# Optimization experiments

Hardware: AMD Instinct MI355X
Metric: run time of the kernel (lower is better)

## Reference

```python
import jax, jax.numpy as jnp
import numpy as np

D, H, DFF, N = 256, 8, 2048, 100
B, T, M1, M2 = 64, 77, 400, 400
DH = D // H
EPS = 1e-5
NEG = -1e9


def _ln(x, w, b):
    m = jnp.mean(x, axis=-1, keepdims=True)
    v = jnp.mean((x - m) ** 2, axis=-1, keepdims=True)
    return (x - m) / jnp.sqrt(v + EPS) * w + b


def _mha(q_in, kv_in, in_w, in_b, out_w, out_b, kpm):
    # q_in: [Tq, D], kv_in: [Tk, D], in_w: [3D, D], kpm: [Tk] bool (True = pad)
    wq, wk, wv = in_w[:D], in_w[D:2 * D], in_w[2 * D:]
    bq, bk, bv = in_b[:D], in_b[D:2 * D], in_b[2 * D:]
    q = (q_in @ wq.T + bq).reshape(-1, H, DH)
    k = (kv_in @ wk.T + bk).reshape(-1, H, DH)
    v = (kv_in @ wv.T + bv).reshape(-1, H, DH)
    scores = jnp.einsum('qhd,khd->hqk', q, k) / np.sqrt(DH).astype(np.float32)
    scores = jnp.where(kpm[None, None, :], NEG, scores)
    attn = jax.nn.softmax(scores, axis=-1)
    out = jnp.einsum('hqk,khd->qhd', attn, v).reshape(-1, D)
    return out @ out_w.T + out_b


def _decoder(x, mem, tmask, mmask, saw, sab, saow, saob,
             caw, cab, caow, caob, l1w, l1b, l2w, l2b,
             n1w, n1b, n2w, n2b, n3w, n3b):
    # Post-norm TransformerDecoderLayer (eval mode, no dropout)
    x = _ln(x + _mha(x, x, saw, sab, saow, saob, tmask), n1w, n1b)
    x = _ln(x + _mha(x, mem, caw, cab, caow, caob, mmask), n2w, n2b)
    ff = jax.nn.relu(x @ l1w.T + l1b) @ l2w.T + l2b
    return _ln(x + ff, n3w, n3b)


def setup_inputs() -> dict:
    key = jax.random.key(0)
    ks = jax.random.split(key, 12)
    s = 0.02
    return {
        'text_embed': jax.random.normal(ks[0], (B, T, D), jnp.float32),
        'text_mask': jnp.zeros((B, T), bool),
        'im_embed1': jax.random.normal(ks[1], (B, M1, D), jnp.float32),
        'im_mask1': jnp.zeros((B, M1), bool),
        'im_embed2': jax.random.normal(ks[2], (B, M2, D), jnp.float32),
        'im_mask2': jnp.zeros((B, M2), bool),
        'sid': jax.random.randint(ks[3], (B,), 0, N),
        'sa_in_w': jax.random.normal(ks[4], (N, 3 * D, D), jnp.float32) * s,
        'sa_in_b': jnp.zeros((N, 3 * D), jnp.float32),
        'sa_out_w': jax.random.normal(ks[5], (N, D, D), jnp.float32) * s,
        'sa_out_b': jnp.zeros((N, D), jnp.float32),
        'ca_in_w': jax.random.normal(ks[6], (N, 3 * D, D), jnp.float32) * s,
        'ca_in_b': jnp.zeros((N, 3 * D), jnp.float32),
        'ca_out_w': jax.random.normal(ks[7], (N, D, D), jnp.float32) * s,
        'ca_out_b': jnp.zeros((N, D), jnp.float32),
        'lin1_w': jax.random.normal(ks[8], (N, DFF, D), jnp.float32) * s,
        'lin1_b': jnp.zeros((N, DFF), jnp.float32),
        'lin2_w': jax.random.normal(ks[9], (N, D, DFF), jnp.float32) * s,
        'lin2_b': jnp.zeros((N, D), jnp.float32),
        'ln1_w': jnp.ones((N, D), jnp.float32),
        'ln1_b': jnp.zeros((N, D), jnp.float32),
        'ln2_w': jnp.ones((N, D), jnp.float32),
        'ln2_b': jnp.zeros((N, D), jnp.float32),
        'ln3_w': jnp.ones((N, D), jnp.float32),
        'ln3_b': jnp.zeros((N, D), jnp.float32),
    }


def reference(text_embed, text_mask, im_embed1, im_mask1, im_embed2, im_mask2, sid,
              sa_in_w, sa_in_b, sa_out_w, sa_out_b,
              ca_in_w, ca_in_b, ca_out_w, ca_out_b,
              lin1_w, lin1_b, lin2_w, lin2_b,
              ln1_w, ln1_b, ln2_w, ln2_b, ln3_w, ln3_b):
    mem = jnp.concatenate([im_embed1, im_embed2], axis=1)    # [B, M1+M2, D]
    mmask = jnp.concatenate([im_mask1, im_mask2], axis=1)    # [B, M1+M2]
    params = tuple(p[sid] for p in (
        sa_in_w, sa_in_b, sa_out_w, sa_out_b,
        ca_in_w, ca_in_b, ca_out_w, ca_out_b,
        lin1_w, lin1_b, lin2_w, lin2_b,
        ln1_w, ln1_b, ln2_w, ln2_b, ln3_w, ln3_b))
    return jax.vmap(_decoder)(text_embed, mem, text_mask, mmask, *params)
```

## Files before the change

kernel.cpp:

```cpp
#include <hip/hip_runtime.h>
#include <hip/hip_bf16.h>
#include <math.h>

constexpr int kB   = 64;
constexpr int kT   = 77;
constexpr int kD   = 256;
constexpr int kH   = 8;
constexpr int kDH  = 32;
constexpr int kDFF = 2048;
constexpr int kM1  = 400;
constexpr int kMKV = 800;
constexpr float kEPS = 1e-5f;
constexpr float kNEG = -1000000000.0f;

typedef __attribute__((ext_vector_type(8))) short short8;
typedef __attribute__((ext_vector_type(4))) float floatx4;

__device__ __forceinline__ unsigned pkbf(float x, float y) {
    unsigned ux = __float_as_uint(x), uy = __float_as_uint(y);
    ux = (ux + 0x7fffu + ((ux >> 16) & 1u)) >> 16;
    uy = (uy + 0x7fffu + ((uy >> 16) & 1u)) & 0xffff0000u;
    return ux | uy;
}

__global__ __launch_bounds__(256) void mfma_gemm(
    const float* __restrict__ A1, long long sA1,
    const float* __restrict__ A2, long long sA2, int splitM, int lda,
    const float* __restrict__ W, long long sW, int ldw,
    const float* __restrict__ bias, long long sB,
    float* __restrict__ C, long long sC, int ldc,
    const int* __restrict__ sid, int M, int N, int K, int tilesM, int relu)
{
    __shared__ unsigned short As[128][88];
    __shared__ unsigned short Bs[128][88];

    int b = blockIdx.z;
    int s = sid[b];
    int ty = blockIdx.x % tilesM;
    int tx = blockIdx.x / tilesM;
    int tm0 = ty * 128, tn0 = tx * 128;

    const float* Wb = W + (long long)s * sW;
    const float* Bb = bias + (long long)s * sB;
    float* Cb = C + (long long)b * sC;

    int t = threadIdx.x;
    int lane = t & 63, wv = t >> 6;
    int wm = wv >> 1, wn = wv & 1;
    int q = lane >> 4, mrow = lane & 15;

    floatx4 acc[4][4] = {};

    for (int k0 = 0; k0 < K; k0 += 64) {
        #pragma unroll
        for (int p = 0; p < 8; p++) {
            int row = (t >> 4) + 16 * p;
            int kf  = (t & 15) * 4;
            int ar = tm0 + row;
            float4 v = make_float4(0.f, 0.f, 0.f, 0.f);
            if (ar < M) {
                const float* src = (ar < splitM)
                    ? (A1 + (long long)b * sA1 + (long long)ar * lda)
                    : (A2 + (long long)b * sA2 + (long long)(ar - splitM) * lda);
                v = *(const float4*)(src + k0 + kf);
            }
            *(uint2*)&As[row][kf] = make_uint2(pkbf(v.x, v.y), pkbf(v.z, v.w));
        }
        #pragma unroll
        for (int p = 0; p < 8; p++) {
            int row = (t >> 4) + 16 * p;
            int kf  = (t & 15) * 4;
            const float* src = Wb + (long long)(tn0 + row) * ldw + k0 + kf;
            float4 v = *(const float4*)src;
            *(uint2*)&Bs[row][kf] = make_uint2(pkbf(v.x, v.y), pkbf(v.z, v.w));
        }
        __syncthreads();

        #pragma unroll
        for (int ks = 0; ks < 2; ks++) {
            int kk = ks * 32 + q * 8;
            short8 af[4], bfr[4];
            #pragma unroll
            for (int i = 0; i < 4; i++) {
                af[i]  = *(const short8*)&As[wm * 64 + i * 16 + mrow][kk];
                bfr[i] = *(const short8*)&Bs[wn * 64 + i * 16 + mrow][kk];
            }
            #pragma unroll
            for (int mi = 0; mi < 4; mi++)
                #pragma unroll
                for (int ni = 0; ni < 4; ni++)
                    acc[mi][ni] = __builtin_amdgcn_mfma_f32_16x16x32_bf16(
                        af[mi], bfr[ni], acc[mi][ni], 0, 0, 0);
        }
        __syncthreads();
    }

    #pragma unroll
    for (int ni = 0; ni < 4; ni++) {
        int cgl = tn0 + wn * 64 + ni * 16 + mrow;
        float bv = Bb[cgl];
        #pragma unroll
        for (int mi = 0; mi < 4; mi++) {
            #pragma unroll
            for (int e = 0; e < 4; e++) {
                int r = tm0 + wm * 64 + mi * 16 + q * 4 + e;
                if (r < M) {
                    float o = acc[mi][ni][e] + bv;
                    if (relu) o = fmaxf(o, 0.f);
                    Cb[(long long)r * ldc + cgl] = o;
                }
            }
        }
    }
}

__global__ __launch_bounds__(256) void attn2(
    const float* __restrict__ Q, long long sQ, int ldq,
    const float* __restrict__ Kp, long long sK, int ldk,
    const float* __restrict__ Vp, long long sV, int ldv,
    const unsigned char* __restrict__ m1, int sM1,
    const unsigned char* __restrict__ m2, int sM2,
    int split, int nk, int ntiles,
    float* __restrict__ O, long long sO, int ldo, float scale)
{
    __shared__ float Ks[64][36];
    __shared__ float Vs[64][36];
    __shared__ float S[32][68];
    __shared__ float mk[64];
    __shared__ float mrowL[32], lrowL[32], alphaL[32];

    int t = threadIdx.x;
    int qt = blockIdx.x, h = blockIdx.y, b = blockIdx.z;
    int qbase = qt * 32;

    const float* Qb = Q + (long long)b * sQ + h * kDH;
    const float* Kb = Kp + (long long)b * sK + h * kDH;
    const float* Vb = Vp + (long long)b * sV + h * kDH;

    int qg = t >> 4, jl = t & 15;
    int r0 = 2 * qg, r1 = r0 + 1;
    int gq0 = qbase + r0, gq1 = qbase + r1;

    float4 qa0[8], qa1[8];
    #pragma unroll
    for (int i = 0; i < 8; i++) {
        qa0[i] = (gq0 < kT) ? *(const float4*)(Qb + (long long)gq0 * ldq + i * 4)
                            : make_float4(0.f, 0.f, 0.f, 0.f);
        qa1[i] = (gq1 < kT) ? *(const float4*)(Qb + (long long)gq1 * ldq + i * 4)
                            : make_float4(0.f, 0.f, 0.f, 0.f);
    }
    float oa00 = 0.f, oa01 = 0.f, oa10 = 0.f, oa11 = 0.f;
    if (t < 32) { mrowL[t] = -INFINITY; lrowL[t] = 0.f; }

    for (int tile = 0; tile < ntiles; tile++) {
        int jt0 = tile * 64;
        __syncthreads();

        #pragma unroll
        for (int p = 0; p < 2; p++) {
            int id = t + 256 * p;
            int j = id >> 3, dq = (id & 7) * 4;
            int gj = jt0 + j;
            float4 kv = (gj < nk) ? *(const float4*)(Kb + (long long)gj * ldk + dq)
                                  : make_float4(0.f, 0.f, 0.f, 0.f);
            float4 vv = (gj < nk) ? *(const float4*)(Vb + (long long)gj * ldv + dq)
                                  : make_float4(0.f, 0.f, 0.f, 0.f);
            *(float4*)&Ks[j][dq] = kv;
            *(float4*)&Vs[j][dq] = vv;
        }
        if (t < 64) {
            int gj = jt0 + t;
            float m = 0.f;
            if (gj < nk)
                m = ((gj < split) ? m1[b * sM1 + gj] : m2[b * sM2 + (gj - split)]) ? 1.f : 0.f;
            mk[t] = m;
        }
        __syncthreads();

        #pragma unroll
        for (int jj = 0; jj < 4; jj++) {
            int j = jl + 16 * jj;
            float a0 = 0.f, a1 = 0.f;
            #pragma unroll
            for (int d4 = 0; d4 < 8; d4++) {
                float4 kv = *(const float4*)&Ks[j][d4 * 4];
                a0 += qa0[d4].x * kv.x + qa0[d4].y * kv.y + qa0[d4].z * kv.z + qa0[d4].w * kv.w;
                a1 += qa1[d4].x * kv.x + qa1[d4].y * kv.y + qa1[d4].z * kv.z + qa1[d4].w * kv.w;
            }
            int gj = jt0 + j;
            float s0, s1;
            if (gj < nk) {
                float msk = mk[j];
                s0 = (msk != 0.f) ? kNEG : a0 * scale;
                s1 = (msk != 0.f) ? kNEG : a1 * scale;
            } else {
                s0 = -INFINITY; s1 = -INFINITY;
            }
            S[r0][j] = s0;
            S[r1][j] = s1;
        }
        __syncthreads();

        if (t < 32) {
            float mo = mrowL[t], lo = lrowL[t];
            float mt = -INFINITY;
            #pragma unroll
            for (int i = 0; i < 16; i++) {
                float4 sv = *(const float4*)&S[t][i * 4];
                mt = fmaxf(mt, fmaxf(fmaxf(sv.x, sv.y), fmaxf(sv.z, sv.w)));
            }
            float mn = fmaxf(mo, mt);
            float al = __expf(mo - mn);
            float ln = lo * al;
            #pragma unroll
            for (int i = 0; i < 16; i++) {
                float4 sv = *(const float4*)&S[t][i * 4];
                sv.x = __expf(sv.x - mn); sv.y = __expf(sv.y - mn);
                sv.z = __expf(sv.z - mn); sv.w = __expf(sv.w - mn);
                ln += sv.x + sv.y + sv.z + sv.w;
                *(float4*)&S[t][i * 4] = sv;
            }
            mrowL[t] = mn; lrowL[t] = ln; alphaL[t] = al;
        }
        __syncthreads();

        float al0 = alphaL[r0], al1 = alphaL[r1];
        oa00 *= al0; oa01 *= al0; oa10 *= al1; oa11 *= al1;
        #pragma unroll
        for (int j4 = 0; j4 < 64; j4 += 4) {
            float4 p0 = *(const float4*)&S[r0][j4];
            float4 p1 = *(const float4*)&S[r1][j4];
            const float* p0a = (const float*)&p0;
            const float* p1a = (const float*)&p1;
            #pragma unroll
            for (int e = 0; e < 4; e++) {
                float2 v = *(const float2*)&Vs[j4 + e][2 * jl];
                oa00 += p0a[e] * v.x; oa01 += p0a[e] * v.y;
                oa10 += p1a[e] * v.x; oa11 += p1a[e] * v.y;
            }
        }
    }

    float li0 = 1.f / lrowL[r0];
    float li1 = 1.f / lrowL[r1];
    if (gq0 < kT) {
        float2 o = make_float2(oa00 * li0, oa01 * li0);
        *(float2*)(O + (long long)b * sO + (long long)gq0 * ldo + h * kDH + 2 * jl) = o;
    }
    if (gq1 < kT) {
        float2 o = make_float2(oa10 * li1, oa11 * li1);
        *(float2*)(O + (long long)b * sO + (long long)gq1 * ldo + h * kDH + 2 * jl) = o;
    }
}

__global__ __launch_bounds__(256) void addln_kernel(
    const float* __restrict__ A, const float* __restrict__ R,
    const float* __restrict__ w, const float* __restrict__ bb,
    const int* __restrict__ sid, float* __restrict__ O)
{
    int t = blockIdx.x, b = blockIdx.y, d = threadIdx.x;
    long long base = ((long long)(b * kT + t)) * kD;
    float x = A[base + d] + R[base + d];

    __shared__ float r1[4], r2[4];
    int wid = d >> 6;

    float sacc = x;
    #pragma unroll
    for (int off = 32; off >= 1; off >>= 1) sacc += __shfl_xor(sacc, off);
    if ((d & 63) == 0) r1[wid] = sacc;
    __syncthreads();
    float mean = (r1[0] + r1[1] + r1[2] + r1[3]) * (1.0f / 256.0f);

    float diff = x - mean;
    float s2 = diff * diff;
    #pragma unroll
    for (int off = 32; off >= 1; off >>= 1) s2 += __shfl_xor(s2, off);
    if ((d & 63) == 0) r2[wid] = s2;
    __syncthreads();
    float var = (r2[0] + r2[1] + r2[2] + r2[3]) * (1.0f / 256.0f);

    int s = sid[b];
    float y = diff * rsqrtf(var + kEPS) * w[s * kD + d] + bb[s * kD + d];
    O[base + d] = y;
}

extern "C" void kernel_launch(void* const* d_in, const int* in_sizes, int n_in,
                              void* d_out, int out_size, void* d_ws, size_t ws_size,
                              hipStream_t stream)
{
    const float*         text   = (const float*)d_in[0];
    const unsigned char* tmask  = (const unsigned char*)d_in[1];
    const float*         im1    = (const float*)d_in[2];
    const unsigned char* immk1  = (const unsigned char*)d_in[3];
    const float*         im2    = (const float*)d_in[4];
    const unsigned char* immk2  = (const unsigned char*)d_in[5];
    const int*           sid    = (const int*)d_in[6];
    const float* sa_in_w  = (const float*)d_in[7];
    const float* sa_in_b  = (const float*)d_in[8];
    const float* sa_out_w = (const float*)d_in[9];
    const float* sa_out_b = (const float*)d_in[10];
    const float* ca_in_w  = (const float*)d_in[11];
    const float* ca_in_b  = (const float*)d_in[12];
    const float* ca_out_w = (const float*)d_in[13];
    const float* ca_out_b = (const float*)d_in[14];
    const float* lin1_w   = (const float*)d_in[15];
    const float* lin1_b   = (const float*)d_in[16];
    const float* lin2_w   = (const float*)d_in[17];
    const float* lin2_b   = (const float*)d_in[18];
    const float* ln1_w    = (const float*)d_in[19];
    const float* ln1_b    = (const float*)d_in[20];
    const float* ln2_w    = (const float*)d_in[21];
    const float* ln2_b    = (const float*)d_in[22];
    const float* ln3_w    = (const float*)d_in[23];
    const float* ln3_b    = (const float*)d_in[24];
    float* out = (float*)d_out;

    float* ws = (float*)d_ws;
    float* qkv_sa  = ws;
    float* q_ca    = qkv_sa  + (long long)kB * kT * 768;
    float* kv_ca   = q_ca    + (long long)kB * kT * kD;
    float* attnbuf = kv_ca   + (long long)kB * kMKV * 512;
    float* tmp     = attnbuf + (long long)kB * kT * kD;
    float* x1      = tmp     + (long long)kB * kT * kD;
    float* x2      = x1      + (long long)kB * kT * kD;
    float* hff     = x2      + (long long)kB * kT * kD;

    const float scale = 0.17677669529663687f;
    dim3 blk(256);

    auto gemm = [&](const float* A1, long long sA1, const float* A2, long long sA2,
                    int splitM, int lda,
                    const float* W, long long sW, int ldw,
                    const float* bias, long long sB,
                    float* C, long long sC, int ldc,
                    int M, int N, int K, int relu) {
        int tm = (M + 127) / 128, tn = N / 128;
        mfma_gemm<<<dim3(tm * tn, 1, kB), blk, 0, stream>>>(
            A1, sA1, A2, sA2, splitM, lda, W, sW, ldw, bias, sB,
            C, sC, ldc, sid, M, N, K, tm, relu);
    };

    gemm(text, (long long)kT * kD, text, 0, kT, kD,
         sa_in_w, (long long)3 * kD * kD, kD, sa_in_b, 3 * kD,
         qkv_sa, (long long)kT * 768, 768, kT, 768, kD, 0);

    attn2<<<dim3(3, kH, kB), blk, 0, stream>>>(
        qkv_sa,       (long long)kT * 768, 768,
        qkv_sa + 256, (long long)kT * 768, 768,
        qkv_sa + 512, (long long)kT * 768, 768,
        tmask, kT, tmask, kT, kT, kT, 2,
        attnbuf, (long long)kT * kD, kD, scale);

    gemm(attnbuf, (long long)kT * kD, attnbuf, 0, kT, kD,
         sa_out_w, (long long)kD * kD, kD, sa_out_b, kD,
         tmp, (long long)kT * kD, kD, kT, kD, kD, 0);

    addln_kernel<<<dim3(kT, kB), blk, 0, stream>>>(tmp, text, ln1_w, ln1_b, sid, x1);

    gemm(x1, (long long)kT * kD, x1, 0, kT, kD,
         ca_in_w, (long long)3 * kD * kD, kD, ca_in_b, 3 * kD,
         q_ca, (long long)kT * kD, kD, kT, kD, kD, 0);

    gemm(im1, (long long)kM1 * kD, im2, (long long)kM1 * kD, kM1, kD,
         ca_in_w + (long long)kD * kD, (long long)3 * kD * kD, kD,
         ca_in_b + kD, 3 * kD,
         kv_ca, (long long)kMKV * 512, 512, kMKV, 512, kD, 0);

    attn2<<<dim3(3, kH, kB), blk, 0, stream>>>(
        q_ca,        (long long)kT * kD, kD,
        kv_ca,       (long long)kMKV * 512, 512,
        kv_ca + 256, (long long)kMKV * 512, 512,
        immk1, kM1, immk2, kM1, kM1, kMKV, 13,
        attnbuf, (long long)kT * kD, kD, scale);

    gemm(attnbuf, (long long)kT * kD, attnbuf, 0, kT, kD,
         ca_out_w, (long long)kD * kD, kD, ca_out_b, kD,
         tmp, (long long)kT * kD, kD, kT, kD, kD, 0);

    addln_kernel<<<dim3(kT, kB), blk, 0, stream>>>(tmp, x1, ln2_w, ln2_b, sid, x2);

    gemm(x2, (long long)kT * kD, x2, 0, kT, kD,
         lin1_w, (long long)kDFF * kD, kD, lin1_b, kDFF,
         hff, (long long)kT * kDFF, kDFF, kT, kDFF, kD, 1);

    gemm(hff, (long long)kT * kDFF, hff, 0, kT, kDFF,
         lin2_w, (long long)kD * kDFF, kDFF, lin2_b, kD,
         tmp, (long long)kT * kD, kD, kT, kD, kDFF, 0);

    addln_kernel<<<dim3(kT, kB), blk, 0, stream>>>(tmp, x2, ln3_w, ln3_b, sid, out);
}
```

Baseline: 1.118 ms.

## Rewrite attention kernel with bf16 MFMA, per-wave split-K softmax and prefetch

Replaces the scalar FP32 attention kernel with one that converts Q, K and V tiles to bf16 in shared memory and computes QK^T and PV with MFMA instructions. Each of the four waves handles its own 16-key slice with a private online softmax, and the partial results are merged through shared memory at the end. The next K/V tile is loaded into registers while the current one is computed, and the separate softmax pass with its extra barriers is removed. This reduces scalar FMA work and synchronization but lowers precision to bf16 for scores and probabilities and adds a cross-wave reduction.

```diff
diff --git a/kernel.cpp b/kernel.cpp
--- a/kernel.cpp
+++ b/kernel.cpp
@@ -15,12 +15,17 @@
 
 typedef __attribute__((ext_vector_type(8))) short short8;
 typedef __attribute__((ext_vector_type(4))) float floatx4;
+typedef __attribute__((ext_vector_type(16))) float floatx16;
 
 __device__ __forceinline__ unsigned pkbf(float x, float y) {
     unsigned ux = __float_as_uint(x), uy = __float_as_uint(y);
     ux = (ux + 0x7fffu + ((ux >> 16) & 1u)) >> 16;
     uy = (uy + 0x7fffu + ((uy >> 16) & 1u)) & 0xffff0000u;
     return ux | uy;
+}
+__device__ __forceinline__ unsigned short bf16u(float x) {
+    unsigned u = __float_as_uint(x);
+    return (unsigned short)((u + 0x7fffu + ((u >> 16) & 1u)) >> 16);
 }
 
 __global__ __launch_bounds__(256) void mfma_gemm(
@@ -114,7 +119,7 @@
     }
 }
 
-__global__ __launch_bounds__(256) void attn2(
+__global__ __launch_bounds__(256) void attn3(
     const float* __restrict__ Q, long long sQ, int ldq,
     const float* __restrict__ Kp, long long sK, int ldk,
     const float* __restrict__ Vp, long long sV, int ldv,
@@ -123,133 +128,170 @@
     int split, int nk, int ntiles,
     float* __restrict__ O, long long sO, int ldo, float scale)
 {
-    __shared__ float Ks[64][36];
-    __shared__ float Vs[64][36];
-    __shared__ float S[32][68];
-    __shared__ float mk[64];
-    __shared__ float mrowL[32], lrowL[32], alphaL[32];
+    __shared__ __align__(16) char smem[19456];
+    unsigned short (*Kl)[40] = (unsigned short (*)[40])(smem);
+    unsigned short (*Vt)[36] = (unsigned short (*)[36])(smem + 5120);
+    unsigned short (*Ql)[40] = (unsigned short (*)[40])(smem + 7424);
+    char* Pbyte = smem + 9984;
+    float* mkf  = (float*)(smem + 16128);
 
     int t = threadIdx.x;
     int qt = blockIdx.x, h = blockIdx.y, b = blockIdx.z;
     int qbase = qt * 32;
 
-    const float* Qb = Q + (long long)b * sQ + h * kDH;
+    const float* Qb = Q  + (long long)b * sQ + h * kDH;
     const float* Kb = Kp + (long long)b * sK + h * kDH;
     const float* Vb = Vp + (long long)b * sV + h * kDH;
 
-    int qg = t >> 4, jl = t & 15;
-    int r0 = 2 * qg, r1 = r0 + 1;
-    int gq0 = qbase + r0, gq1 = qbase + r1;
-
-    float4 qa0[8], qa1[8];
+    int lane = t & 63, w = t >> 6;
+    int lq = lane & 15, q4 = lane >> 4;
+    int d31 = lane & 31, hh = lane >> 5;
+    int sj = t >> 2, sd = (t & 3) * 8;
+
+    {
+        int q = t >> 3, df = (t & 7) * 4;
+        int gq = qbase + q;
+        float4 v = make_float4(0.f, 0.f, 0.f, 0.f);
+        if (gq < kT) v = *(const float4*)(Qb + (long long)gq * ldq + df);
+        *(uint2*)&Ql[q][df] = make_uint2(pkbf(v.x, v.y), pkbf(v.z, v.w));
+    }
+
+    float4 ka, kb, va, vb; float mkv = 0.f;
+    auto issue_loads = [&](int jt) {
+        int gj = jt + sj;
+        if (gj < nk) {
+            const float* kp = Kb + (long long)gj * ldk + sd;
+            const float* vp = Vb + (long long)gj * ldv + sd;
+            ka = *(const float4*)kp;  kb = *(const float4*)(kp + 4);
+            va = *(const float4*)vp;  vb = *(const float4*)(vp + 4);
+        } else {
+            ka = kb = va = vb = make_float4(0.f, 0.f, 0.f, 0.f);
+        }
+        if (t < 64) {
+            int tj = jt + t;
+            if (tj < nk)
+                mkv = ((tj < split) ? m1[b * sM1 + tj] : m2[b * sM2 + (tj - split)])
+                        ? kNEG : 0.f;
+            else
+                mkv = -INFINITY;
+        }
+    };
+    auto write_stage = [&]() {
+        *(uint4*)&Kl[sj][sd] = make_uint4(pkbf(ka.x, ka.y), pkbf(ka.z, ka.w),
+                                          pkbf(kb.x, kb.y), pkbf(kb.z, kb.w));
+        Vt[sd + 0][sj] = bf16u(va.x); Vt[sd + 1][sj] = bf16u(va.y);
+        Vt[sd + 2][sj] = bf16u(va.z); Vt[sd + 3][sj] = bf16u(va.w);
+        Vt[sd + 4][sj] = bf16u(vb.x); Vt[sd + 5][sj] = bf16u(vb.y);
+        Vt[sd + 6][sj] = bf16u(vb.z); Vt[sd + 7][sj] = bf16u(vb.w);
+        if (t < 64) mkf[t] = mkv;
+    };
+
+    issue_loads(0);
+    write_stage();
+    __syncthreads();
+
+    short8 Bq0 = *(const short8*)&Ql[lq][8 * q4];
+    short8 Bq1 = *(const short8*)&Ql[lq + 16][8 * q4];
+
+    floatx16 accO = {};
+    float m0 = -INFINITY, m1v = -INFINITY, l0 = 0.f, l1 = 0.f;
+    char* Pw = Pbyte + w * 1536;
+
+    for (int tile = 0; tile < ntiles; tile++) {
+        bool pf = (tile + 1 < ntiles);
+        if (pf) issue_loads((tile + 1) * 64);
+
+        short8 akf = *(const short8*)&Kl[16 * w + lq][8 * q4];
+        floatx4 c0 = {}, c1 = {};
+        c0 = __builtin_amdgcn_mfma_f32_16x16x32_bf16(akf, Bq0, c0, 0, 0, 0);
+        c1 = __builtin_amdgcn_mfma_f32_16x16x32_bf16(akf, Bq1, c1, 0, 0, 0);
+
+        float mka0 = mkf[16 * w + 4 * q4 + 0];
+        float mka1 = mkf[16 * w + 4 * q4 + 1];
+        float mka2 = mkf[16 * w + 4 * q4 + 2];
+        float mka3 = mkf[16 * w + 4 * q4 + 3];
+
+        float s00 = c0[0] * scale + mka0, s01 = c0[1] * scale + mka1;
+        float s02 = c0[2] * scale + mka2, s03 = c0[3] * scale + mka3;
+        float s10 = c1[0] * scale + mka0, s11 = c1[1] * scale + mka1;
+        float s12 = c1[2] * scale + mka2, s13 = c1[3] * scale + mka3;
+
+        float mt0 = fmaxf(fmaxf(s00, s01), fmaxf(s02, s03));
+        float mt1 = fmaxf(fmaxf(s10, s11), fmaxf(s12, s13));
+        mt0 = fmaxf(mt0, __shfl_xor(mt0, 16)); mt0 = fmaxf(mt0, __shfl_xor(mt0, 32));
+        mt1 = fmaxf(mt1, __shfl_xor(mt1, 16)); mt1 = fmaxf(mt1, __shfl_xor(mt1, 32));
+        float mn0 = fmaxf(m0, mt0), mn1 = fmaxf(m1v, mt1);
+        float al0 = __expf(m0 - mn0), al1 = __expf(m1v - mn1);
+
+        float p00 = __expf(s00 - mn0), p01 = __expf(s01 - mn0);
+        float p02 = __expf(s02 - mn0), p03 = __expf(s03 - mn0);
+        float p10 = __expf(s10 - mn1), p11 = __expf(s11 - mn1);
+        float p12 = __expf(s12 - mn1), p13 = __expf(s13 - mn1);
+
+        float sum0 = (p00 + p01) + (p02 + p03);
+        float sum1 = (p10 + p11) + (p12 + p13);
+        sum0 += __shfl_xor(sum0, 16); sum0 += __shfl_xor(sum0, 32);
+        sum1 += __shfl_xor(sum1, 16); sum1 += __shfl_xor(sum1, 32);
+        l0 = l0 * al0 + sum0;  l1 = l1 * al1 + sum1;
+        m0 = mn0;  m1v = mn1;
+
+        *(unsigned*)(Pw + lq * 48 + (8 * q4 + 0))        = pkbf(p00, p01);
+        *(unsigned*)(Pw + lq * 48 + (8 * q4 + 4))        = pkbf(p02, p03);
+        *(unsigned*)(Pw + (lq + 16) * 48 + ((8 * q4 + 0) ^ 16)) = pkbf(p10, p11);
+        *(unsigned*)(Pw + (lq + 16) * 48 + ((8 * q4 + 4) ^ 16)) = pkbf(p12, p13);
+        short8 bp = *(const short8*)(Pw + d31 * 48 + ((16 * hh) ^ (d31 & 16)));
+
+        int j0 = 16 * w + 8 * hh;
+        uint2 va2 = *(const uint2*)&Vt[d31][j0];
+        uint2 vb2 = *(const uint2*)&Vt[d31][j0 + 4];
+        union { unsigned u[4]; short8 s; } avu;
+        avu.u[0] = va2.x; avu.u[1] = va2.y; avu.u[2] = vb2.x; avu.u[3] = vb2.y;
+
+        float als = (lane & 16) ? al1 : al0;
+        #pragma unroll
+        for (int e = 0; e < 16; e++) accO[e] *= als;
+        accO = __builtin_amdgcn_mfma_f32_32x32x16_bf16(avu.s, bp, accO, 0, 0, 0);
+
+        __syncthreads();
+        if (pf) { write_stage(); __syncthreads(); }
+    }
+
+    float* Ow = (float*)smem;
+    float* ms = (float*)(smem + 18432);
+    float* ls = (float*)(smem + 18944);
     #pragma unroll
-    for (int i = 0; i < 8; i++) {
-        qa0[i] = (gq0 < kT) ? *(const float4*)(Qb + (long long)gq0 * ldq + i * 4)
-                            : make_float4(0.f, 0.f, 0.f, 0.f);
-        qa1[i] = (gq1 < kT) ? *(const float4*)(Qb + (long long)gq1 * ldq + i * 4)
-                            : make_float4(0.f, 0.f, 0.f, 0.f);
-    }
-    float oa00 = 0.f, oa01 = 0.f, oa10 = 0.f, oa11 = 0.f;
-    if (t < 32) { mrowL[t] = -INFINITY; lrowL[t] = 0.f; }
-
-    for (int tile = 0; tile < ntiles; tile++) {
-        int jt0 = tile * 64;
-        __syncthreads();
-
-        #pragma unroll
-        for (int p = 0; p < 2; p++) {
-            int id = t + 256 * p;
-            int j = id >> 3, dq = (id & 7) * 4;
-            int gj = jt0 + j;
-            float4 kv = (gj < nk) ? *(const float4*)(Kb + (long long)gj * ldk + dq)
-                                  : make_float4(0.f, 0.f, 0.f, 0.f);
-            float4 vv = (gj < nk) ? *(const float4*)(Vb + (long long)gj * ldv + dq)
-                                  : make_float4(0.f, 0.f, 0.f, 0.f);
-            *(float4*)&Ks[j][dq] = kv;
-            *(float4*)&Vs[j][dq] = vv;
-        }
-        if (t < 64) {
-            int gj = jt0 + t;
-            float m = 0.f;
-            if (gj < nk)
-                m = ((gj < split) ? m1[b * sM1 + gj] : m2[b * sM2 + (gj - split)]) ? 1.f : 0.f;
-            mk[t] = m;
-        }
-        __syncthreads();
-
-        #pragma unroll
-        for (int jj = 0; jj < 4; jj++) {
-            int j = jl + 16 * jj;
-            float a0 = 0.f, a1 = 0.f;
-            #pragma unroll
-            for (int d4 = 0; d4 < 8; d4++) {
-                float4 kv = *(const float4*)&Ks[j][d4 * 4];
-                a0 += qa0[d4].x * kv.x + qa0[d4].y * kv.y + qa0[d4].z * kv.z + qa0[d4].w * kv.w;
-                a1 += qa1[d4].x * kv.x + qa1[d4].y * kv.y + qa1[d4].z * kv.z + qa1[d4].w * kv.w;
-            }
-            int gj = jt0 + j;
-            float s0, s1;
-            if (gj < nk) {
-                float msk = mk[j];
-                s0 = (msk != 0.f) ? kNEG : a0 * scale;
-                s1 = (msk != 0.f) ? kNEG : a1 * scale;
-            } else {
-                s0 = -INFINITY; s1 = -INFINITY;
-            }
-            S[r0][j] = s0;
-            S[r1][j] = s1;
-        }
-        __syncthreads();
-
-        if (t < 32) {
-            float mo = mrowL[t], lo = lrowL[t];
-            float mt = -INFINITY;
-            #pragma unroll
-            for (int i = 0; i < 16; i++) {
-                float4 sv = *(const float4*)&S[t][i * 4];
-                mt = fmaxf(mt, fmaxf(fmaxf(sv.x, sv.y), fmaxf(sv.z, sv.w)));
-            }
-            float mn = fmaxf(mo, mt);
-            float al = __expf(mo - mn);
-            float ln = lo * al;
-            #pragma unroll
-            for (int i = 0; i < 16; i++) {
-                float4 sv = *(const float4*)&S[t][i * 4];
-                sv.x = __expf(sv.x - mn); sv.y = __expf(sv.y - mn);
-                sv.z = __expf(sv.z - mn); sv.w = __expf(sv.w - mn);
-                ln += sv.x + sv.y + sv.z + sv.w;
-                *(float4*)&S[t][i * 4] = sv;
-            }
-            mrowL[t] = mn; lrowL[t] = ln; alphaL[t] = al;
-        }
-        __syncthreads();
-
-        float al0 = alphaL[r0], al1 = alphaL[r1];
-        oa00 *= al0; oa01 *= al0; oa10 *= al1; oa11 *= al1;
-        #pragma unroll
-        for (int j4 = 0; j4 < 64; j4 += 4) {
-            float4 p0 = *(const float4*)&S[r0][j4];
-            float4 p1 = *(const float4*)&S[r1][j4];
-            const float* p0a = (const float*)&p0;
-            const float* p1a = (const float*)&p1;
-            #pragma unroll
-            for (int e = 0; e < 4; e++) {
-                float2 v = *(const float2*)&Vs[j4 + e][2 * jl];
-                oa00 += p0a[e] * v.x; oa01 += p0a[e] * v.y;
-                oa10 += p1a[e] * v.x; oa11 += p1a[e] * v.y;
-            }
-        }
-    }
-
-    float li0 = 1.f / lrowL[r0];
-    float li1 = 1.f / lrowL[r1];
-    if (gq0 < kT) {
-        float2 o = make_float2(oa00 * li0, oa01 * li0);
-        *(float2*)(O + (long long)b * sO + (long long)gq0 * ldo + h * kDH + 2 * jl) = o;
-    }
-    if (gq1 < kT) {
-        float2 o = make_float2(oa10 * li1, oa11 * li1);
-        *(float2*)(O + (long long)b * sO + (long long)gq1 * ldo + h * kDH + 2 * jl) = o;
+    for (int g = 0; g < 4; g++) {
+        int d0 = 8 * g + 4 * hh;
+        float4 ve = make_float4(accO[4 * g + 0], accO[4 * g + 1],
+                                accO[4 * g + 2], accO[4 * g + 3]);
+        *(float4*)&Ow[(w * 32 + d31) * 36 + d0] = ve;
+    }
+    if (q4 == 0) {
+        ms[w * 32 + lq] = m0;   ms[w * 32 + lq + 16] = m1v;
+        ls[w * 32 + lq] = l0;   ls[w * 32 + lq + 16] = l1;
+    }
+    __syncthreads();
+    {
+        int qq = t >> 3, db = (t & 7) * 4;
+        float mw0 = ms[qq],      mw1 = ms[32 + qq];
+        float mw2 = ms[64 + qq], mw3 = ms[96 + qq];
+        float M = fmaxf(fmaxf(mw0, mw1), fmaxf(mw2, mw3));
+        float e0 = __expf(mw0 - M), e1 = __expf(mw1 - M);
+        float e2 = __expf(mw2 - M), e3 = __expf(mw3 - M);
+        float L = e0 * ls[qq] + e1 * ls[32 + qq] + e2 * ls[64 + qq] + e3 * ls[96 + qq];
+        float inv = 1.f / L;
+        float4 o0 = *(const float4*)&Ow[(0 * 32 + qq) * 36 + db];
+        float4 o1 = *(const float4*)&Ow[(1 * 32 + qq) * 36 + db];
+        float4 o2 = *(const float4*)&Ow[(2 * 32 + qq) * 36 + db];
+        float4 o3 = *(const float4*)&Ow[(3 * 32 + qq) * 36 + db];
+        float4 o;
+        o.x = (e0 * o0.x + e1 * o1.x + e2 * o2.x + e3 * o3.x) * inv;
+        o.y = (e0 * o0.y + e1 * o1.y + e2 * o2.y + e3 * o3.y) * inv;
+        o.z = (e0 * o0.z + e1 * o1.z + e2 * o2.z + e3 * o3.z) * inv;
+        o.w = (e0 * o0.w + e1 * o1.w + e2 * o2.w + e3 * o3.w) * inv;
+        int gq = qbase + qq;
+        if (gq < kT)
+            *(float4*)(O + (long long)b * sO + (long long)gq * ldo + h * kDH + db) = o;
     }
 }
 
@@ -345,7 +387,7 @@
          sa_in_w, (long long)3 * kD * kD, kD, sa_in_b, 3 * kD,
          qkv_sa, (long long)kT * 768, 768, kT, 768, kD, 0);
 
-    attn2<<<dim3(3, kH, kB), blk, 0, stream>>>(
+    attn3<<<dim3(3, kH, kB), blk, 0, stream>>>(
         qkv_sa,       (long long)kT * 768, 768,
         qkv_sa + 256, (long long)kT * 768, 768,
         qkv_sa + 512, (long long)kT * 768, 768,
@@ -367,7 +409,7 @@
          ca_in_b + kD, 3 * kD,
          kv_ca, (long long)kMKV * 512, 512, kMKV, 512, kD, 0);
 
-    attn2<<<dim3(3, kH, kB), blk, 0, stream>>>(
+    attn3<<<dim3(3, kH, kB), blk, 0, stream>>>(
         q_ca,        (long long)kT * kD, kD,
         kv_ca,       (long long)kMKV * 512, 512,
         kv_ca + 256, (long long)kMKV * 512, 512,
```

Result: faster. 1.006 ms (-10.0%).
